# Kernel optimization log

Measured on AMD Instinct MI355X. Metric: run time of the kernel, lower is better.

The kernel has to match this reference:

```python
import jax, jax.numpy as jnp
import numpy as np

DIM = 1024
H = 16
HD = DIM // H  # 64
BASE = 10000.0


def _rope_tables(seq_len, d):
    # freqs over half-dim, then TILED (repeat) along last axis as in the torch code
    freqs = 1.0 / (BASE ** (jnp.arange(0, d, 2, dtype=jnp.float32) / d))  # [d/2]
    t = jnp.arange(seq_len, dtype=jnp.float32)
    f = jnp.outer(t, freqs)  # [S, d/2]
    cos = jnp.concatenate([jnp.cos(f), jnp.cos(f)], axis=-1)  # [S, d] (tiled, NOT interleaved)
    sin = jnp.concatenate([jnp.sin(f), jnp.sin(f)], axis=-1)
    return cos, sin


def _apply_rope(x):
    # x: [B, H, S, d]; rotation pairs adjacent elements (2i, 2i+1)
    S, d = x.shape[-2], x.shape[-1]
    cos, sin = _rope_tables(S, d)  # [S, d]
    xh = x.reshape(*x.shape[:-1], d // 2, 2)
    x_rot = jnp.stack([-xh[..., 1], xh[..., 0]], axis=-1).reshape(x.shape)
    return x * cos + x_rot * sin


def setup_inputs() -> dict:
    key = jax.random.key(0)
    ks = jax.random.split(key, 7)
    B, Sq, Sk = 16, 512, 512
    s = 0.02
    return {
        "x": jax.random.normal(ks[0], (B, Sq, DIM), jnp.float32),
        "context": jax.random.normal(ks[1], (B, Sk, DIM), jnp.float32),
        "Wq": jax.random.normal(ks[2], (DIM, DIM), jnp.float32) * s,
        "Wk": jax.random.normal(ks[3], (DIM, DIM), jnp.float32) * s,
        "Wv": jax.random.normal(ks[4], (DIM, DIM), jnp.float32) * s,
        "Wo": jax.random.normal(ks[5], (DIM, DIM), jnp.float32) * s,
        "bo": jax.random.normal(ks[6], (DIM,), jnp.float32) * s,
    }


def reference(x, context, Wq, Wk, Wv, Wo, bo):
    B, Sq, _ = x.shape
    Sk = context.shape[1]
    scale = HD ** -0.5
    # projections, split heads: [B, H, S, HD]
    q = (x @ Wq).reshape(B, Sq, H, HD).transpose(0, 2, 1, 3)
    k = (context @ Wk).reshape(B, Sk, H, HD).transpose(0, 2, 1, 3)
    v = (context @ Wv).reshape(B, Sk, H, HD).transpose(0, 2, 1, 3)
    q = _apply_rope(q)
    k = _apply_rope(k)
    attn = jax.nn.softmax(jnp.einsum("bhqd,bhkd->bhqk", q, k) * scale, axis=-1)
    out = jnp.einsum("bhqk,bhkd->bhqd", attn, v)
    out = out.transpose(0, 2, 1, 3).reshape(B, Sq, DIM)
    return out @ Wo + bo  # dropout is identity (p=0 / eval)
```

## Files before the change

### kernel.cpp

```cpp
#include <hip/hip_runtime.h>

#define DIM   1024
#define NH    16
#define HD    64
#define BATCH 16
#define SEQ   512
#define MROWS (BATCH*SEQ)
#define SL2E  0.18033688011112042f

typedef __bf16 bf16x8 __attribute__((ext_vector_type(8)));
typedef float  floatx4 __attribute__((ext_vector_type(4)));
typedef short  short4v __attribute__((ext_vector_type(4)));

static __device__ __forceinline__ unsigned short f2bf(float f) {
    union { float f; unsigned u; } v; v.f = f;
    return (unsigned short)((v.u + 0x8000u) >> 16);
}
static __device__ __forceinline__ unsigned pk2(float a, float b) {
    union { float f; unsigned u; } x, y; x.f = a; y.f = b;
    return ((x.u + 0x8000u) >> 16) | ((y.u + 0x8000u) & 0xffff0000u);
}

static __device__ __forceinline__ void glds16(const void* g, void* l) {
    __builtin_amdgcn_global_load_lds(
        (const __attribute__((address_space(1))) unsigned int*)g,
        (__attribute__((address_space(3))) unsigned int*)l, 16, 0, 0);
}

__global__ __launch_bounds__(256)
void prep(const float* __restrict__ x, const float* __restrict__ ctx,
          const float* __restrict__ Wq, const float* __restrict__ Wk,
          const float* __restrict__ Wv, const float* __restrict__ Wo,
          unsigned short* __restrict__ xb, unsigned short* __restrict__ cb,
          unsigned short* __restrict__ WqT, unsigned short* __restrict__ WkT,
          unsigned short* __restrict__ WvT, unsigned short* __restrict__ WoT,
          float2* __restrict__ cstab)
{
    __shared__ float tile[32][33];
    const int blk = blockIdx.x, t = threadIdx.x;
    if (blk < 8192) {
        const float* src = (blk < 4096) ? x : ctx;
        unsigned short* dst = (blk < 4096) ? xb : cb;
        int e = ((blk & 4095) * 256 + t) * 8;
        float4 f0 = *(const float4*)&src[e];
        float4 f1 = *(const float4*)&src[e + 4];
        uint4 o = { pk2(f0.x, f0.y), pk2(f0.z, f0.w), pk2(f1.x, f1.y), pk2(f1.z, f1.w) };
        *(uint4*)&dst[e] = o;
    } else if (blk < 12288) {
        int id2 = blk - 8192;
        const float* W; unsigned short* T;
        switch (id2 >> 10) {
            case 0:  W = Wq; T = WqT; break;
            case 1:  W = Wk; T = WkT; break;
            case 2:  W = Wv; T = WvT; break;
            default: W = Wo; T = WoT; break;
        }
        int local = id2 & 1023;
        int n0 = (local & 31) * 32, k0 = (local >> 5) * 32;
        int tx = t & 31, ty = t >> 5;
        #pragma unroll
        for (int a = 0; a < 4; a++)
            tile[ty + 8 * a][tx] = W[(size_t)(k0 + ty + 8 * a) * DIM + n0 + tx];
        __syncthreads();
        #pragma unroll
        for (int a = 0; a < 4; a++)
            T[(size_t)(n0 + ty + 8 * a) * DIM + k0 + tx] = f2bf(tile[tx][ty + 8 * a]);
    } else {
        int gid = (blk - 12288) * 256 + t;
        int d = gid & (HD - 1), s = gid >> 6;
        const float C = -0.41524101186092f;
        float f = exp2f((float)(d & 31) * C);
        float a = (float)s * f;
        cstab[gid] = make_float2(cosf(a), sinf(a));
    }
}

static __device__ __forceinline__ void gemm_main(
    const unsigned short* __restrict__ A, const unsigned short* __restrict__ Bt,
    int m0, int n0, unsigned short* As, unsigned short* Bs, floatx4 acc[4][4])
{
    const int t = threadIdx.x;
    const int w = t >> 6, l = t & 63;
    const int wm = w >> 1, wn = w & 1;
    const int lane16 = l & 15, quad = l >> 4;
    const int lr = l >> 3, lc = (l & 7) * 8;

    #pragma unroll
    for (int mi = 0; mi < 4; mi++)
        #pragma unroll
        for (int ni = 0; ni < 4; ni++) acc[mi][ni] = (floatx4){0.f, 0.f, 0.f, 0.f};

    for (int kt = 0; kt < DIM; kt += 64) {
        #pragma unroll
        for (int j = 0; j < 4; j++) {
            int ch = w * 4 + j;
            int row = ch * 8 + lr;
            glds16(A  + (size_t)(m0 + row) * DIM + kt + lc, &As[ch * 512]);
            glds16(Bt + (size_t)(n0 + row) * DIM + kt + lc, &Bs[ch * 512]);
        }
        __syncthreads();
        #pragma unroll
        for (int kk = 0; kk < 2; kk++) {
            bf16x8 af[4], bfr[4];
            #pragma unroll
            for (int mi = 0; mi < 4; mi++)
                af[mi] = *(const bf16x8*)&As[(wm * 64 + mi * 16 + lane16) * 64 + kk * 32 + quad * 8];
            #pragma unroll
            for (int ni = 0; ni < 4; ni++)
                bfr[ni] = *(const bf16x8*)&Bs[(wn * 64 + ni * 16 + lane16) * 64 + kk * 32 + quad * 8];
            #pragma unroll
            for (int mi = 0; mi < 4; mi++)
                #pragma unroll
                for (int ni = 0; ni < 4; ni++)
                    acc[mi][ni] = __builtin_amdgcn_mfma_f32_16x16x32_bf16(bfr[ni], af[mi], acc[mi][ni], 0, 0, 0);
        }
        __syncthreads();
    }
}

static __device__ __forceinline__ void proj_epilogue(
    unsigned short* __restrict__ Out, const float2* __restrict__ cstab,
    int m0, int n0, int mode, floatx4 acc[4][4])
{
    const int t = threadIdx.x;
    const int w = t >> 6, l = t & 63;
    const int wm = w >> 1, wn = w & 1;
    const int lane16 = l & 15, quad = l >> 4;

    if (mode == 0) {
        #pragma unroll
        for (int mi = 0; mi < 4; mi++) {
            int m = m0 + wm * 64 + mi * 16 + lane16;
            int s = m & 511, b = m >> 9;
            #pragma unroll
            for (int ni = 0; ni < 4; ni++) {
                int n = n0 + wn * 64 + ni * 16 + quad * 4;
                int h = n >> 6, d0 = n & 63;
                const float4* cp = (const float4*)&cstab[s * HD + d0];
                float4 c01 = cp[0];
                float4 c23 = cp[1];
                floatx4 v = acc[mi][ni];
                float r0 = v[0] * c01.x - v[1] * c01.y;
                float r1 = fmaf(v[0], c01.w, v[1] * c01.z);
                float r2 = v[2] * c23.x - v[3] * c23.y;
                float r3 = fmaf(v[2], c23.w, v[3] * c23.z);
                uint2 o = { pk2(r0, r1), pk2(r2, r3) };
                *(uint2*)&Out[((size_t)(b * NH + h) * SEQ + s) * HD + d0] = o;
            }
        }
    } else {
        #pragma unroll
        for (int mi = 0; mi < 4; mi++) {
            int m = m0 + wm * 64 + mi * 16 + lane16;
            #pragma unroll
            for (int ni = 0; ni < 4; ni++) {
                int n = n0 + wn * 64 + ni * 16 + quad * 4;
                floatx4 v = acc[mi][ni];
                uint2 o = { pk2(v[0], v[1]), pk2(v[2], v[3]) };
                *(uint2*)&Out[((size_t)(n >> 9) * DIM + m) * SEQ + (n & 511)] = o;
            }
        }
    }
}

__global__ __launch_bounds__(256)
void proj_kv(const unsigned short* __restrict__ cb,
             const unsigned short* __restrict__ WkT, const unsigned short* __restrict__ WvT,
             unsigned short* __restrict__ Kb, unsigned short* __restrict__ Vtb,
             const float2* __restrict__ cstab)
{
    __shared__ unsigned short As[128 * 64];
    __shared__ unsigned short Bs[128 * 64];
    const unsigned short *A, *Bt; unsigned short* Out;
    int m0, n0, mode;
    int id = blockIdx.x;
    if (id < 512) { A = cb;  Bt = WkT; Out = Kb;  mode = 0; n0 = (id & 7) * 128; m0 = (id >> 3) * 128; }
    else { int i2 = id - 512;
           A = WvT; Bt = cb;  Out = Vtb; mode = 1; m0 = (i2 & 7) * 128; n0 = (i2 >> 3) * 128; }
    floatx4 acc[4][4];
    gemm_main(A, Bt, m0, n0, As, Bs, acc);
    proj_epilogue(Out, cstab, m0, n0, mode, acc);
}

__global__ __launch_bounds__(256)
void proj_q(const unsigned short* __restrict__ xb, const unsigned short* __restrict__ WqT,
            unsigned short* __restrict__ Qb, const float2* __restrict__ cstab)
{
    __shared__ unsigned short As[128 * 64];
    __shared__ unsigned short Bs[128 * 64];
    int id = blockIdx.x;
    int n0 = (id & 7) * 128, m0 = (id >> 3) * 128;
    floatx4 acc[4][4];
    gemm_main(xb, WqT, m0, n0, As, Bs, acc);
    proj_epilogue(Qb, cstab, m0, n0, 0, acc);
}

__global__ __launch_bounds__(256)
void out_gemm(const unsigned short* __restrict__ Ab, const unsigned short* __restrict__ WoT,
              float* __restrict__ O, const float* __restrict__ bias)
{
    __shared__ unsigned short As[128 * 64];
    __shared__ unsigned short Bs[128 * 64];
    int id = blockIdx.x;
    int n0 = (id & 7) * 128, m0 = (id >> 3) * 128;
    floatx4 acc[4][4];
    gemm_main(Ab, WoT, m0, n0, As, Bs, acc);

    const int t = threadIdx.x;
    const int w = t >> 6, l = t & 63;
    const int wm = w >> 1, wn = w & 1;
    const int lane16 = l & 15, quad = l >> 4;
    #pragma unroll
    for (int ni = 0; ni < 4; ni++) {
        int n = n0 + wn * 64 + ni * 16 + quad * 4;
        float4 bv = *(const float4*)&bias[n];
        #pragma unroll
        for (int mi = 0; mi < 4; mi++) {
            int m = m0 + wm * 64 + mi * 16 + lane16;
            floatx4 v = acc[mi][ni];
            float4 o = { v[0] + bv.x, v[1] + bv.y, v[2] + bv.z, v[3] + bv.w };
            *(float4*)&O[(size_t)m * DIM + n] = o;
        }
    }
}

__global__ __launch_bounds__(256, 4)
void attn_v4(const unsigned short* __restrict__ Q, const unsigned short* __restrict__ K,
             const unsigned short* __restrict__ Vt, unsigned short* __restrict__ Out)
{
    __shared__ unsigned short Qs[128][72];
    __shared__ unsigned short Ks[64][72];
    __shared__ unsigned short Vts[64][72];

    const int id = blockIdx.x;
    const int qi = (id >> 3) & 3;
    const int bh = (id & 7) | ((id >> 5) << 3);
    const int q0 = qi * 128;
    const int t  = threadIdx.x;
    const int w = t >> 6, l = t & 63;
    const int lane16 = l & 15, quad = l >> 4;
    const size_t base = (size_t)bh * SEQ * HD;

    const int sr = t >> 3, sc = (t & 7) * 8;
    #pragma unroll
    for (int j = 0; j < 4; j++)
        *(uint4*)&Qs[j * 32 + sr][sc] =
            *(const uint4*)&Q[base + (size_t)(q0 + j * 32 + sr) * HD + sc];

    const unsigned short* kp0 = K  + base + (size_t)sr * HD + sc;
    const unsigned short* kp1 = kp0 + (size_t)32 * HD;
    const unsigned short* vp0 = Vt + base + (size_t)sr * SEQ + sc;
    const unsigned short* vp1 = vp0 + (size_t)32 * SEQ;

    floatx4 acc_o[2][4];
    float lsum[2] = {0.f, 0.f};
    #pragma unroll
    for (int st = 0; st < 2; st++)
        #pragma unroll
        for (int dt = 0; dt < 4; dt++) acc_o[st][dt] = (floatx4){0.f, 0.f, 0.f, 0.f};

    for (int kt = 0; kt < SEQ; kt += 64) {
        __syncthreads();
        *(uint4*)&Ks[sr][sc]       = *(const uint4*)kp0;  kp0 += 64 * HD;
        *(uint4*)&Ks[sr + 32][sc]  = *(const uint4*)kp1;  kp1 += 64 * HD;
        *(uint4*)&Vts[sr][sc]      = *(const uint4*)vp0;  vp0 += 64;
        *(uint4*)&Vts[sr + 32][sc] = *(const uint4*)vp1;  vp1 += 64;
        __syncthreads();

        bf16x8 kf[2][4];
        #pragma unroll
        for (int kk = 0; kk < 2; kk++)
            #pragma unroll
            for (int c = 0; c < 4; c++)
                kf[kk][c] = *(const bf16x8*)&Ks[c * 16 + lane16][kk * 32 + quad * 8];

        short4v pa[2][4];
        #pragma unroll
        for (int st = 0; st < 2; st++) {
            floatx4 sacc[4];
            #pragma unroll
            for (int c = 0; c < 4; c++) sacc[c] = (floatx4){0.f, 0.f, 0.f, 0.f};
            #pragma unroll
            for (int kk = 0; kk < 2; kk++) {
                bf16x8 qf = *(const bf16x8*)&Qs[st * 64 + w * 16 + lane16][kk * 32 + quad * 8];
                #pragma unroll
                for (int c = 0; c < 4; c++)
                    sacc[c] = __builtin_amdgcn_mfma_f32_16x16x32_bf16(kf[kk][c], qf, sacc[c], 0, 0, 0);
            }
            #pragma unroll
            for (int c = 0; c < 4; c++) {
                short4v pk;
                #pragma unroll
                for (int i = 0; i < 4; i++) {
                    float pv = exp2f(sacc[c][i] * SL2E);
                    lsum[st] += pv;
                    pk[i] = (short)f2bf(pv);
                }
                pa[st][c] = pk;
            }
        }
        #pragma unroll
        for (int c = 0; c < 4; c++) {
            #pragma unroll
            for (int dt = 0; dt < 4; dt++) {
                short4v vf = *(const short4v*)&Vts[dt * 16 + lane16][c * 16 + quad * 4];
                #pragma unroll
                for (int st = 0; st < 2; st++)
                    acc_o[st][dt] = __builtin_amdgcn_mfma_f32_16x16x16bf16_1k(
                        vf, pa[st][c], acc_o[st][dt], 0, 0, 0);
            }
        }
    }

    const int b = bh >> 4, h = bh & 15;
    #pragma unroll
    for (int st = 0; st < 2; st++) {
        float rs = lsum[st];
        rs += __shfl_xor(rs, 16, 64);
        rs += __shfl_xor(rs, 32, 64);
        float inv = 1.0f / rs;
        int s = q0 + st * 64 + w * 16 + lane16;
        size_t rowbase = (size_t)(b * SEQ + s) * DIM + h * HD;
        #pragma unroll
        for (int dt = 0; dt < 4; dt++) {
            floatx4 v = acc_o[st][dt];
            uint2 o = { pk2(v[0] * inv, v[1] * inv), pk2(v[2] * inv, v[3] * inv) };
            *(uint2*)&Out[rowbase + dt * 16 + quad * 4] = o;
        }
    }
}

extern "C" void kernel_launch(void* const* d_in, const int* in_sizes, int n_in,
                              void* d_out, int out_size, void* d_ws, size_t ws_size,
                              hipStream_t stream)
{
    const float* x   = (const float*)d_in[0];
    const float* ctx = (const float*)d_in[1];
    const float* Wq  = (const float*)d_in[2];
    const float* Wk  = (const float*)d_in[3];
    const float* Wv  = (const float*)d_in[4];
    const float* Wo  = (const float*)d_in[5];
    const float* bo  = (const float*)d_in[6];

    const size_t NW = (size_t)DIM * DIM;
    const size_t NB = (size_t)MROWS * DIM;

    unsigned short* x_bf   = (unsigned short*)d_ws;
    unsigned short* ctx_bf = x_bf + NB;
    unsigned short* WqT    = ctx_bf + NB;
    unsigned short* WkT    = WqT + NW;
    unsigned short* WvT    = WkT + NW;
    unsigned short* WoT    = WvT + NW;
    unsigned short* Kb     = WoT + NW;
    unsigned short* Vtb    = Kb + NB;
    float2*         cstab  = (float2*)(Vtb + NB);
    unsigned short* Qb     = ctx_bf;
    unsigned short* Ab     = x_bf;

    prep<<<12416, 256, 0, stream>>>(x, ctx, Wq, Wk, Wv, Wo,
                                    x_bf, ctx_bf, WqT, WkT, WvT, WoT, cstab);

    proj_kv<<<1024, 256, 0, stream>>>(ctx_bf, WkT, WvT, Kb, Vtb, cstab);
    proj_q<<<512, 256, 0, stream>>>(x_bf, WqT, Qb, cstab);

    attn_v4<<<1024, 256, 0, stream>>>(Qb, Kb, Vtb, Ab);

    out_gemm<<<512, 256, 0, stream>>>(Ab, WoT, (float*)d_out, bo);
}
```

Measured before the change: 292.0 us.

## Swizzle GEMM LDS layout, merge Q/K/V projections, and remap blocks per XCD

The GEMM tile loads now XOR-swizzle the 16-byte column chunk by row, both in the global-to-LDS copy and in the fragment reads, so the bf16x8 LDS reads stop hitting the same banks. The K/V and Q projection kernels are merged into a single 1536-block launch, which drops one launch and lets Q tiles fill the machine alongside K/V. Block indices are remapped so consecutive blocks that share an A row-panel land on the same XCD, aiming for better L2 reuse. Q is now staged in the output buffer instead of the context buffer, since the merged kernel still reads context while Q is written.

```diff
diff --git a/kernel.cpp b/kernel.cpp
--- a/kernel.cpp
+++ b/kernel.cpp
@@ -83,31 +83,36 @@
     const int w = t >> 6, l = t & 63;
     const int wm = w >> 1, wn = w & 1;
     const int lane16 = l & 15, quad = l >> 4;
-    const int lr = l >> 3, lc = (l & 7) * 8;
+    const int lr = l >> 3;
+    const int gsw = ((l & 7) ^ lr) * 8;
+    const int co0 = (quad ^ (lane16 & 7)) * 8;
+    const int co1 = co0 ^ 32;
 
     #pragma unroll
     for (int mi = 0; mi < 4; mi++)
         #pragma unroll
         for (int ni = 0; ni < 4; ni++) acc[mi][ni] = (floatx4){0.f, 0.f, 0.f, 0.f};
 
+    const unsigned short* ap = A  + (size_t)(m0 + w * 32 + lr) * DIM + gsw;
+    const unsigned short* bp = Bt + (size_t)(n0 + w * 32 + lr) * DIM + gsw;
+
     for (int kt = 0; kt < DIM; kt += 64) {
         #pragma unroll
         for (int j = 0; j < 4; j++) {
-            int ch = w * 4 + j;
-            int row = ch * 8 + lr;
-            glds16(A  + (size_t)(m0 + row) * DIM + kt + lc, &As[ch * 512]);
-            glds16(Bt + (size_t)(n0 + row) * DIM + kt + lc, &Bs[ch * 512]);
+            glds16(ap + (size_t)j * 8 * DIM + kt, &As[(w * 4 + j) * 512]);
+            glds16(bp + (size_t)j * 8 * DIM + kt, &Bs[(w * 4 + j) * 512]);
         }
         __syncthreads();
         #pragma unroll
         for (int kk = 0; kk < 2; kk++) {
+            const int co = kk ? co1 : co0;
             bf16x8 af[4], bfr[4];
             #pragma unroll
             for (int mi = 0; mi < 4; mi++)
-                af[mi] = *(const bf16x8*)&As[(wm * 64 + mi * 16 + lane16) * 64 + kk * 32 + quad * 8];
+                af[mi] = *(const bf16x8*)&As[(wm * 64 + mi * 16 + lane16) * 64 + co];
             #pragma unroll
             for (int ni = 0; ni < 4; ni++)
-                bfr[ni] = *(const bf16x8*)&Bs[(wn * 64 + ni * 16 + lane16) * 64 + kk * 32 + quad * 8];
+                bfr[ni] = *(const bf16x8*)&Bs[(wn * 64 + ni * 16 + lane16) * 64 + co];
             #pragma unroll
             for (int mi = 0; mi < 4; mi++)
                 #pragma unroll
@@ -164,45 +169,39 @@
 }
 
 __global__ __launch_bounds__(256)
-void proj_kv(const unsigned short* __restrict__ cb,
-             const unsigned short* __restrict__ WkT, const unsigned short* __restrict__ WvT,
-             unsigned short* __restrict__ Kb, unsigned short* __restrict__ Vtb,
-             const float2* __restrict__ cstab)
+void proj_qkv(const unsigned short* __restrict__ xb, const unsigned short* __restrict__ cb,
+              const unsigned short* __restrict__ WqT, const unsigned short* __restrict__ WkT,
+              const unsigned short* __restrict__ WvT,
+              unsigned short* __restrict__ Qb, unsigned short* __restrict__ Kb,
+              unsigned short* __restrict__ Vtb, const float2* __restrict__ cstab)
 {
     __shared__ unsigned short As[128 * 64];
     __shared__ unsigned short Bs[128 * 64];
+    const int id = blockIdx.x;
+    const int seg = id >> 9, local = id & 511;
+    const int xcd = local & 7, seq = local >> 3;
     const unsigned short *A, *Bt; unsigned short* Out;
     int m0, n0, mode;
-    int id = blockIdx.x;
-    if (id < 512) { A = cb;  Bt = WkT; Out = Kb;  mode = 0; n0 = (id & 7) * 128; m0 = (id >> 3) * 128; }
-    else { int i2 = id - 512;
-           A = WvT; Bt = cb;  Out = Vtb; mode = 1; m0 = (i2 & 7) * 128; n0 = (i2 >> 3) * 128; }
+    if (seg == 0)      { A = cb;  Bt = WkT; Out = Kb;  mode = 0;
+                         n0 = (seq & 7) * 128; m0 = (xcd + 8 * (seq >> 3)) * 128; }
+    else if (seg == 1) { A = WvT; Bt = cb;  Out = Vtb; mode = 1;
+                         m0 = (seq & 7) * 128; n0 = (xcd + 8 * (seq >> 3)) * 128; }
+    else               { A = xb;  Bt = WqT; Out = Qb;  mode = 0;
+                         n0 = (seq & 7) * 128; m0 = (xcd + 8 * (seq >> 3)) * 128; }
     floatx4 acc[4][4];
     gemm_main(A, Bt, m0, n0, As, Bs, acc);
     proj_epilogue(Out, cstab, m0, n0, mode, acc);
 }
 
 __global__ __launch_bounds__(256)
-void proj_q(const unsigned short* __restrict__ xb, const unsigned short* __restrict__ WqT,
-            unsigned short* __restrict__ Qb, const float2* __restrict__ cstab)
+void out_gemm(const unsigned short* __restrict__ Ab, const unsigned short* __restrict__ WoT,
+              float* __restrict__ O, const float* __restrict__ bias)
 {
     __shared__ unsigned short As[128 * 64];
     __shared__ unsigned short Bs[128 * 64];
-    int id = blockIdx.x;
-    int n0 = (id & 7) * 128, m0 = (id >> 3) * 128;
-    floatx4 acc[4][4];
-    gemm_main(xb, WqT, m0, n0, As, Bs, acc);
-    proj_epilogue(Qb, cstab, m0, n0, 0, acc);
-}
-
-__global__ __launch_bounds__(256)
-void out_gemm(const unsigned short* __restrict__ Ab, const unsigned short* __restrict__ WoT,
-              float* __restrict__ O, const float* __restrict__ bias)
-{
-    __shared__ unsigned short As[128 * 64];
-    __shared__ unsigned short Bs[128 * 64];
-    int id = blockIdx.x;
-    int n0 = (id & 7) * 128, m0 = (id >> 3) * 128;
+    const int id = blockIdx.x;
+    const int xcd = id & 7, seq = id >> 3;
+    const int n0 = (seq & 7) * 128, m0 = (xcd + 8 * (seq >> 3)) * 128;
     floatx4 acc[4][4];
     gemm_main(Ab, WoT, m0, n0, As, Bs, acc);
 
@@ -354,14 +353,14 @@
     unsigned short* Kb     = WoT + NW;
     unsigned short* Vtb    = Kb + NB;
     float2*         cstab  = (float2*)(Vtb + NB);
-    unsigned short* Qb     = ctx_bf;
+    unsigned short* Qb     = (unsigned short*)d_out;
     unsigned short* Ab     = x_bf;
 
     prep<<<12416, 256, 0, stream>>>(x, ctx, Wq, Wk, Wv, Wo,
                                     x_bf, ctx_bf, WqT, WkT, WvT, WoT, cstab);
 
-    proj_kv<<<1024, 256, 0, stream>>>(ctx_bf, WkT, WvT, Kb, Vtb, cstab);
-    proj_q<<<512, 256, 0, stream>>>(x_bf, WqT, Qb, cstab);
+    proj_qkv<<<1536, 256, 0, stream>>>(x_bf, ctx_bf, WqT, WkT, WvT,
+                                       Qb, Kb, Vtb, cstab);
 
     attn_v4<<<1024, 256, 0, stream>>>(Qb, Kb, Vtb, Ab);
 
```

Result: faster. 262.7 us (-10.0%).
